# Kernel optimization log

Hardware: AMD Instinct MI355X
Metric: run time of the kernel (lower is better)

The kernel has to match this reference:

```python
import jax, jax.numpy as jnp
import numpy as np

N = 50000
E = 1600000
IN = 128
HID = 128
OUT = 64
NL = 200000
NEG_SLOPE = 0.2


def _glorot(key, shape):
    fan_in, fan_out = shape[0], shape[-1]
    s = jnp.sqrt(6.0 / (fan_in + fan_out))
    return jax.random.uniform(key, shape, jnp.float32, -s, s)


def setup_inputs() -> dict:
    key = jax.random.key(0)
    ks = jax.random.split(key, 16)
    x = jax.random.normal(ks[0], (N, IN), jnp.float32)
    edge_index = jax.random.randint(ks[1], (2, E), 0, N, dtype=jnp.int32)
    edge_label_index = jax.random.randint(ks[2], (2, NL), 0, N, dtype=jnp.int32)
    return {
        "x": x,
        "edge_index": edge_index,
        "edge_label_index": edge_label_index,
        "W1": _glorot(ks[3], (IN, HID)),  "a1s": _glorot(ks[4], (HID,)),  "a1d": _glorot(ks[5], (HID,)),  "b1": jnp.zeros((HID,), jnp.float32),
        "W2": _glorot(ks[6], (HID, HID)), "a2s": _glorot(ks[7], (HID,)),  "a2d": _glorot(ks[8], (HID,)),  "b2": jnp.zeros((HID,), jnp.float32),
        "W3": _glorot(ks[9], (HID, HID)), "a3s": _glorot(ks[10], (HID,)), "a3d": _glorot(ks[11], (HID,)), "b3": jnp.zeros((HID,), jnp.float32),
        "W4": _glorot(ks[12], (HID, OUT)), "b4": jnp.zeros((OUT,), jnp.float32),
    }


def _add_self_loops(edge_index, n):
    loop = jnp.arange(n, dtype=edge_index.dtype)
    return jnp.concatenate([edge_index, jnp.stack([loop, loop])], axis=1)


def gat_conv(x, edge_index, W, a_s, a_d, b):
    """PyG GATConv, heads=1, add_self_loops=True: gather, LeakyReLU score,
    segment softmax over destination nodes, scatter-add aggregate."""
    n = x.shape[0]
    ei = _add_self_loops(edge_index, n)
    src, dst = ei[0], ei[1]
    h = x @ W                                    # [N, H]
    e = jax.nn.leaky_relu((h @ a_s)[src] + (h @ a_d)[dst], NEG_SLOPE)  # [E']
    m = jax.ops.segment_max(e, dst, num_segments=n)
    p = jnp.exp(e - m[dst])
    s = jax.ops.segment_sum(p, dst, num_segments=n)
    alpha = p / s[dst]                           # segment softmax
    out = jax.ops.segment_sum(h[src] * alpha[:, None], dst, num_segments=n)
    return out + b


def gcn_conv(x, edge_index, W, b):
    """PyG GCNConv: self-loops + symmetric degree normalization."""
    n = x.shape[0]
    ei = _add_self_loops(edge_index, n)
    src, dst = ei[0], ei[1]
    h = x @ W
    deg = jax.ops.segment_sum(jnp.ones(src.shape, h.dtype), dst, num_segments=n)
    dinv = jax.lax.rsqrt(deg)
    norm = dinv[src] * dinv[dst]                 # [E']
    out = jax.ops.segment_sum(h[src] * norm[:, None], dst, num_segments=n)
    return out + b


def reference(x, edge_index, edge_label_index,
              W1, a1s, a1d, b1, W2, a2s, a2d, b2,
              W3, a3s, a3d, b3, W4, b4):
    h = jax.nn.relu(gat_conv(x, edge_index, W1, a1s, a1d, b1))
    h = jax.nn.relu(gat_conv(h, edge_index, W2, a2s, a2d, b2))
    h = jax.nn.relu(gat_conv(h, edge_index, W3, a3s, a3d, b3))
    z = gcn_conv(h, edge_index, W4, b4)          # [N, OUT]
    # decode: dot product of endpoint embeddings -> link logits [NL]
    return (z[edge_label_index[0]] * z[edge_label_index[1]]).sum(axis=-1)
```

## Files before the change

kernel.cpp:

```cpp
#include <hip/hip_runtime.h>
#include <hip/hip_fp16.h>
#include <math.h>

#define NN   50000
#define NE   1600000
#define DHID 128
#define DOUTC 64
#define NLBL 200000
#define CAP  80
#define NEG  0.2f
#define NBK  196
#define CAPB 8800
#define CHK  4096

typedef unsigned short u16;
typedef _Float16 half8 __attribute__((ext_vector_type(8)));
typedef float floatx4 __attribute__((ext_vector_type(4)));


__global__ __launch_bounds__(256) void k_zero(int* __restrict__ gcnt) {
    int i = threadIdx.x;
    if (i < NBK) gcnt[i] = 0;
}

__global__ __launch_bounds__(256) void k_bin(const int* __restrict__ ei,
                                             int* __restrict__ gcnt,
                                             unsigned* __restrict__ bins) {
    __shared__ int cntL[NBK];
    __shared__ int curL[NBK];
    const int tid = threadIdx.x;
    const int e0 = blockIdx.x * CHK + tid * 16;
    const bool act = (e0 + 15) < NE;

    unsigned pk[16];
    int bb[16];
    if (act) {
#pragma unroll
        for (int g = 0; g < 4; ++g) {
            int4 s4 = *(const int4*)&ei[e0 + g * 4];
            int4 d4 = *(const int4*)&ei[NE + e0 + g * 4];
            int sa[4] = {s4.x, s4.y, s4.z, s4.w};
            int da[4] = {d4.x, d4.y, d4.z, d4.w};
#pragma unroll
            for (int k = 0; k < 4; ++k) {
                int idx = g * 4 + k;
                bb[idx] = da[k] >> 8;
                pk[idx] = (unsigned)sa[k] | ((unsigned)(da[k] & 255) << 16);
            }
        }
    }
    for (int i = tid; i < NBK; i += 256) cntL[i] = 0;
    __syncthreads();
    if (act) {
#pragma unroll
        for (int k = 0; k < 16; ++k) atomicAdd(&cntL[bb[k]], 1);
    }
    __syncthreads();
    for (int i = tid; i < NBK; i += 256) curL[i] = atomicAdd(&gcnt[i], cntL[i]);
    __syncthreads();
    if (act) {
#pragma unroll
        for (int k = 0; k < 16; ++k) {
            int off = atomicAdd(&curL[bb[k]], 1);
            bins[(size_t)bb[k] * CAPB + off] = pk[k];
        }
    }
}

__global__ __launch_bounds__(256) void k_build(const unsigned* __restrict__ bins,
                                               const int* __restrict__ gcnt,
                                               int* __restrict__ cnt,
                                               u16* __restrict__ csr) {
    __shared__ u16 rows[256 * CAP];
    __shared__ int cur[256];
    const int b = blockIdx.x, tid = threadIdx.x;
    const int d0 = b << 8;
    const int nd = min(256, NN - d0);
    if (tid < nd) { cur[tid] = 1; rows[tid * CAP] = (u16)(d0 + tid); }
    __syncthreads();
    const int n = gcnt[b];
    for (int i = tid; i < n; i += 256) {
        unsigned v = bins[(size_t)b * CAPB + i];
        int s = v & 0xFFFF, dl = v >> 16;
        int pos = atomicAdd(&cur[dl], 1);
        if (pos < CAP) rows[dl * CAP + pos] = (u16)s;
    }
    __syncthreads();
    const unsigned* rw = (const unsigned*)rows;
    unsigned* cw = (unsigned*)(csr + (size_t)d0 * CAP);
    const int tot = nd * (CAP / 2);
    for (int i = tid; i < tot; i += 256) cw[i] = rw[i];
    if (tid < nd) cnt[d0 + tid] = cur[tid];
}


__global__ __launch_bounds__(256) void k_cast(const float* __restrict__ x,
                                              __half* __restrict__ x16) {
    int i = (blockIdx.x * 256 + threadIdx.x) * 4;
    if (i < NN * 128) {
        float4 v = *(const float4*)&x[i];
        __half2 h0 = __floats2half2_rn(v.x, v.y);
        __half2 h1 = __floats2half2_rn(v.z, v.w);
        uint2 u;
        __builtin_memcpy(&u.x, &h0, 4);
        __builtin_memcpy(&u.y, &h1, 4);
        *(uint2*)&x16[i] = u;
    }
}


__global__ __launch_bounds__(256) void k_prep_w(const float* __restrict__ W1f,
                                                const float* __restrict__ W2f,
                                                const float* __restrict__ W3f,
                                                const float* __restrict__ W4f,
                                                half8* __restrict__ Wf1,
                                                half8* __restrict__ Wf2,
                                                half8* __restrict__ Wf3,
                                                half8* __restrict__ Wf4) {
    int e = blockIdx.x * 256 + threadIdx.x;
    const float* W;
    half8* Wf;
    int nout, le;
    if (e < 2048)      { W = W1f; Wf = Wf1; nout = 128; le = e; }
    else if (e < 4096) { W = W2f; Wf = Wf2; nout = 128; le = e - 2048; }
    else if (e < 6144) { W = W3f; Wf = Wf3; nout = 128; le = e - 4096; }
    else if (e < 7168) { W = W4f; Wf = Wf4; nout = 64;  le = e - 6144; }
    else return;
    int c = le >> 8, rem = le & 255, ks = rem >> 6, lane = rem & 63;
    int n = lane & 15, quad = lane >> 4;
    int col = c * 16 + n, k0 = ks * 32 + quad * 8;
    half8 v;
#pragma unroll
    for (int j = 0; j < 8; ++j) v[j] = (_Float16)W[(size_t)(k0 + j) * nout + col];
    Wf[le] = v;
}


template <int NOUT, bool ATTN>
__global__ __launch_bounds__(256) void gemm_mfma(const __half* __restrict__ A16,
                                                 const half8* __restrict__ Wf,
                                                 __half* __restrict__ C16,
                                                 const float* __restrict__ a_s,
                                                 const float* __restrict__ a_d,
                                                 float* __restrict__ asv,
                                                 float* __restrict__ adv, int M) {
    constexpr int CT = NOUT / 16;
    const int tid = threadIdx.x;
    const int wave = tid >> 6, lane = tid & 63;
    const int n = lane & 15, quad = lane >> 4;
    const int row0 = blockIdx.x * 128 + wave * 32;

    half8 a[2][4];
    half8 zz = {};
#pragma unroll
    for (int t = 0; t < 2; ++t) {
        int row = row0 + t * 16 + n;
        const _Float16* Ap = (const _Float16*)A16 + (size_t)row * 128 + quad * 8;
        bool ok = row < M;
#pragma unroll
        for (int ks = 0; ks < 4; ++ks)
            a[t][ks] = ok ? *(const half8*)(Ap + ks * 32) : zz;
    }

    floatx4 acc[2][CT];
#pragma unroll
    for (int t = 0; t < 2; ++t)
#pragma unroll
        for (int c = 0; c < CT; ++c) acc[t][c] = (floatx4){0.f, 0.f, 0.f, 0.f};

#pragma unroll
    for (int c = 0; c < CT; ++c) {
#pragma unroll
        for (int ks = 0; ks < 4; ++ks) {
            half8 b = Wf[(c * 4 + ks) * 64 + lane];
            acc[0][c] = __builtin_amdgcn_mfma_f32_16x16x32_f16(b, a[0][ks], acc[0][c], 0, 0, 0);
            acc[1][c] = __builtin_amdgcn_mfma_f32_16x16x32_f16(b, a[1][ks], acc[1][c], 0, 0, 0);
        }
    }

#pragma unroll
    for (int t = 0; t < 2; ++t) {
        int row = row0 + t * 16 + n;
        if (row < M) {
#pragma unroll
            for (int c = 0; c < CT; ++c) {
                __half2 h0 = __floats2half2_rn(acc[t][c][0], acc[t][c][1]);
                __half2 h1 = __floats2half2_rn(acc[t][c][2], acc[t][c][3]);
                uint2 u;
                __builtin_memcpy(&u.x, &h0, 4);
                __builtin_memcpy(&u.y, &h1, 4);
                *(uint2*)&C16[(size_t)row * NOUT + c * 16 + quad * 4] = u;
            }
        }
    }

    if (ATTN) {
#pragma unroll
        for (int t = 0; t < 2; ++t) {
            float ps = 0.f, pd = 0.f;
#pragma unroll
            for (int c = 0; c < CT; ++c) {
#pragma unroll
                for (int reg = 0; reg < 4; ++reg) {
                    float w = acc[t][c][reg];
                    ps = fmaf(w, a_s[c * 16 + quad * 4 + reg], ps);
                    pd = fmaf(w, a_d[c * 16 + quad * 4 + reg], pd);
                }
            }
            ps += __shfl_xor(ps, 16); ps += __shfl_xor(ps, 32);
            pd += __shfl_xor(pd, 16); pd += __shfl_xor(pd, 32);
            int row = row0 + t * 16 + n;
            if (quad == 0 && row < M) { asv[row] = ps; adv[row] = pd; }
        }
    }
}

__device__ inline void fma_h8(uint4 u, float al, float* acc) {
    float2 f0 = __half22float2(*(__half2*)&u.x);
    float2 f1 = __half22float2(*(__half2*)&u.y);
    float2 f2 = __half22float2(*(__half2*)&u.z);
    float2 f3 = __half22float2(*(__half2*)&u.w);
    acc[0] = fmaf(al, f0.x, acc[0]);
    acc[1] = fmaf(al, f0.y, acc[1]);
    acc[2] = fmaf(al, f1.x, acc[2]);
    acc[3] = fmaf(al, f1.y, acc[3]);
    acc[4] = fmaf(al, f2.x, acc[4]);
    acc[5] = fmaf(al, f2.y, acc[5]);
    acc[6] = fmaf(al, f3.x, acc[6]);
    acc[7] = fmaf(al, f3.y, acc[7]);
}


__global__ __launch_bounds__(256) void k_gat_agg(const __half* __restrict__ h,
                                                 const int* __restrict__ cnt,
                                                 const u16* __restrict__ csr,
                                                 const float* __restrict__ asv,
                                                 const float* __restrict__ adv,
                                                 const float* __restrict__ bias,
                                                 __half* __restrict__ outp) {
    int lane = threadIdx.x & 63, wv = threadIdx.x >> 6;
    int d = blockIdx.x * 4 + wv;
    if (d >= NN) return;
    int deg = cnt[d]; if (deg > CAP) deg = CAP;
    const float advd = adv[d];
    const u16* rowp = csr + (size_t)d * CAP;

    int j0 = lane, j1 = lane + 64;
    int s0 = 0, s1 = 0;
    float e0 = -INFINITY, e1 = -INFINITY;
    if (j0 < deg) {
        s0 = rowp[j0];
        float t = asv[s0] + advd;
        e0 = (t >= 0.f) ? t : NEG * t;
    }
    if (j1 < deg) {
        s1 = rowp[j1];
        float t = asv[s1] + advd;
        e1 = (t >= 0.f) ? t : NEG * t;
    }
    float m = fmaxf(e0, e1);
#pragma unroll
    for (int off = 32; off; off >>= 1) m = fmaxf(m, __shfl_xor(m, off));
    float p0 = (j0 < deg) ? __expf(e0 - m) : 0.f;
    float p1 = (j1 < deg) ? __expf(e1 - m) : 0.f;
    float s = p0 + p1;
#pragma unroll
    for (int off = 32; off; off >>= 1) s += __shfl_xor(s, off);
    float inv = 1.f / s;
    float a0 = p0 * inv, a1 = p1 * inv;

    int slot = lane >> 3, r = lane & 7;
    float acc[16];
#pragma unroll
    for (int k = 0; k < 16; ++k) acc[k] = 0.f;

    for (int base = 0; base < deg; base += 8) {
        int idx = base + slot;
        int lsrc = idx & 63;
        float alA = __shfl(a0, lsrc);
        float alB = __shfl(a1, lsrc);
        int   sjA = __shfl(s0, lsrc);
        int   sjB = __shfl(s1, lsrc);
        bool ok = idx < deg;
        float al = ok ? ((idx < 64) ? alA : alB) : 0.f;
        int   sj = ok ? ((idx < 64) ? sjA : sjB) : 0;
        const uint4* hp = (const uint4*)&h[(size_t)sj * 128 + r * 16];
        uint4 ua = hp[0];
        uint4 ub = hp[1];
        fma_h8(ua, al, acc);
        fma_h8(ub, al, acc + 8);
    }
#pragma unroll
    for (int k = 0; k < 16; ++k) {
        acc[k] += __shfl_xor(acc[k], 8);
        acc[k] += __shfl_xor(acc[k], 16);
        acc[k] += __shfl_xor(acc[k], 32);
    }
    if (slot == 0) {
        __half2 ho[8];
#pragma unroll
        for (int k = 0; k < 8; ++k) {
            float oa = fmaxf(acc[2 * k]     + bias[r * 16 + 2 * k],     0.f);
            float ob = fmaxf(acc[2 * k + 1] + bias[r * 16 + 2 * k + 1], 0.f);
            ho[k] = __floats2half2_rn(oa, ob);
        }
        uint4 u0, u1;
        __builtin_memcpy(&u0, &ho[0], 16);
        __builtin_memcpy(&u1, &ho[4], 16);
        uint4* op = (uint4*)&outp[(size_t)d * 128 + r * 16];
        op[0] = u0; op[1] = u1;
    }
}


__global__ __launch_bounds__(256) void k_gcn_agg(const __half* __restrict__ h,
                                                 const int* __restrict__ cnt,
                                                 const u16* __restrict__ csr,
                                                 const float* __restrict__ bias,
                                                 float* __restrict__ z) {
    int lane = threadIdx.x & 63, wv = threadIdx.x >> 6;
    int d = blockIdx.x * 4 + wv;
    if (d >= NN) return;
    int degc = cnt[d];
    int deg = degc > CAP ? CAP : degc;
    float did = rsqrtf((float)degc);
    const u16* rowp = csr + (size_t)d * CAP;

    int j0 = lane, j1 = lane + 64;
    int s0 = 0, s1 = 0;
    float n0 = 0.f, n1 = 0.f;
    if (j0 < deg) { s0 = rowp[j0]; n0 = rsqrtf((float)cnt[s0]) * did; }
    if (j1 < deg) { s1 = rowp[j1]; n1 = rsqrtf((float)cnt[s1]) * did; }

    int slot = lane >> 3, r = lane & 7;
    float acc[8];
#pragma unroll
    for (int k = 0; k < 8; ++k) acc[k] = 0.f;

    for (int base = 0; base < deg; base += 8) {
        int idx = base + slot;
        int lsrc = idx & 63;
        float nA = __shfl(n0, lsrc);
        float nB = __shfl(n1, lsrc);
        int  sjA = __shfl(s0, lsrc);
        int  sjB = __shfl(s1, lsrc);
        bool ok = idx < deg;
        float nm = ok ? ((idx < 64) ? nA : nB) : 0.f;
        int   sj = ok ? ((idx < 64) ? sjA : sjB) : 0;
        uint4 u = *(const uint4*)&h[(size_t)sj * 64 + r * 8];
        fma_h8(u, nm, acc);
    }
#pragma unroll
    for (int k = 0; k < 8; ++k) {
        acc[k] += __shfl_xor(acc[k], 8);
        acc[k] += __shfl_xor(acc[k], 16);
        acc[k] += __shfl_xor(acc[k], 32);
    }
    if (slot == 0) {
        float4 b0 = *(const float4*)&bias[r * 8];
        float4 b1 = *(const float4*)&bias[r * 8 + 4];
        float4* zp = (float4*)&z[(size_t)d * 64 + r * 8];
        zp[0] = make_float4(acc[0] + b0.x, acc[1] + b0.y, acc[2] + b0.z, acc[3] + b0.w);
        zp[1] = make_float4(acc[4] + b1.x, acc[5] + b1.y, acc[6] + b1.z, acc[7] + b1.w);
    }
}


__global__ __launch_bounds__(256) void k_decode(const float* __restrict__ z,
                                                const int* __restrict__ eli,
                                                float* __restrict__ outp) {
    int lane = threadIdx.x & 63, wv = threadIdx.x >> 6;
    int g = lane >> 4, r = lane & 15;
    int idx = (blockIdx.x * 4 + wv) * 4 + g;
    if (idx >= NLBL) return;
    int a = eli[idx], b = eli[NLBL + idx];
    float4 za = *(const float4*)&z[(size_t)a * 64 + r * 4];
    float4 zb = *(const float4*)&z[(size_t)b * 64 + r * 4];
    float v = za.x * zb.x + za.y * zb.y + za.z * zb.z + za.w * zb.w;
#pragma unroll
    for (int off = 8; off; off >>= 1) v += __shfl_xor(v, off);
    if (r == 0) outp[idx] = v;
}


extern "C" void kernel_launch(void* const* d_in, const int* in_sizes, int n_in,
                              void* d_out, int out_size, void* d_ws, size_t ws_size,
                              hipStream_t stream) {
    const float* x   = (const float*)d_in[0];
    const int*   ei  = (const int*)d_in[1];
    const int*   eli = (const int*)d_in[2];
    const float* W1 = (const float*)d_in[3];
    const float* a1s = (const float*)d_in[4];
    const float* a1d = (const float*)d_in[5];
    const float* b1 = (const float*)d_in[6];
    const float* W2 = (const float*)d_in[7];
    const float* a2s = (const float*)d_in[8];
    const float* a2d = (const float*)d_in[9];
    const float* b2 = (const float*)d_in[10];
    const float* W3 = (const float*)d_in[11];
    const float* a3s = (const float*)d_in[12];
    const float* a3d = (const float*)d_in[13];
    const float* b3 = (const float*)d_in[14];
    const float* W4 = (const float*)d_in[15];
    const float* b4 = (const float*)d_in[16];
    float* outp = (float*)d_out;

    char* p = (char*)d_ws;
    auto alloc = [&](size_t bytes) -> char* {
        char* r = p;
        p += (bytes + 255) & ~(size_t)255;
        return r;
    };
    int*    cnt  = (int*)alloc((size_t)NN * 4);
    u16*    csr  = (u16*)alloc((size_t)NN * CAP * 2);
    int*    gcnt = (int*)alloc((size_t)NBK * 4);
    float*  asv  = (float*)alloc((size_t)NN * 4);
    float*  advv = (float*)alloc((size_t)NN * 4);
    __half* x16  = (__half*)alloc((size_t)NN * 128 * 2);
    __half* G    = (__half*)alloc((size_t)NN * 128 * 2);
    __half* Bu1  = (__half*)alloc((size_t)NN * 128 * 2);
    __half* Bu2  = (__half*)alloc((size_t)NN * 128 * 2);
    float*  zf   = (float*)alloc((size_t)NN * 64 * 4);
    half8*  Wf1  = (half8*)alloc(2048 * 16);
    half8*  Wf2  = (half8*)alloc(2048 * 16);
    half8*  Wf3  = (half8*)alloc(2048 * 16);
    half8*  Wf4  = (half8*)alloc(1024 * 16);
    unsigned* bins = (unsigned*)alloc((size_t)NBK * CAPB * 4);

    const int gBin  = (NE + CHK - 1) / CHK;
    const int gCast = (NN * 128 / 4 + 255) / 256;
    const int gGemm = (NN + 127) / 128;
    const int gNode = (NN + 3) / 4;
    const int gDec  = (NLBL + 15) / 16;

    k_zero<<<1, 256, 0, stream>>>(gcnt);
    k_bin<<<gBin, 256, 0, stream>>>(ei, gcnt, bins);
    k_build<<<NBK, 256, 0, stream>>>(bins, gcnt, cnt, csr);
    k_cast<<<gCast, 256, 0, stream>>>(x, x16);
    k_prep_w<<<28, 256, 0, stream>>>(W1, W2, W3, W4, Wf1, Wf2, Wf3, Wf4);

    gemm_mfma<128, true><<<gGemm, 256, 0, stream>>>(x16, Wf1, G, a1s, a1d, asv, advv, NN);
    k_gat_agg<<<gNode, 256, 0, stream>>>(G, cnt, csr, asv, advv, b1, Bu1);

    gemm_mfma<128, true><<<gGemm, 256, 0, stream>>>(Bu1, Wf2, G, a2s, a2d, asv, advv, NN);
    k_gat_agg<<<gNode, 256, 0, stream>>>(G, cnt, csr, asv, advv, b2, Bu2);

    gemm_mfma<128, true><<<gGemm, 256, 0, stream>>>(Bu2, Wf3, G, a3s, a3d, asv, advv, NN);
    k_gat_agg<<<gNode, 256, 0, stream>>>(G, cnt, csr, asv, advv, b3, Bu1);

    gemm_mfma<64, false><<<gGemm, 256, 0, stream>>>(Bu1, Wf4, G, nullptr, nullptr, nullptr, nullptr, NN);
    k_gcn_agg<<<gNode, 256, 0, stream>>>(G, cnt, csr, b4, zf);

    k_decode<<<gDec, 256, 0, stream>>>(zf, eli, outp);
}
```

Baseline: 430.2 us.

## Fuse cast into first GEMM, merge zero kernel, use LDS edge lists, fp16 z

The fp32→fp16 cast of x moves into the first GEMM through a templated input type, and the gcnt zeroing is folded into k_prep_w as an extra block, which removes two launches and one full pass over x. The GEMM now does 16 rows per wave instead of 32, which doubles the grid and reduces register pressure. The GAT and GCN aggregations stage per-edge alpha/norm and source indices in LDS instead of using per-iteration shuffles. The final embedding z is stored in fp16, halving decode gather traffic at some precision cost.

```diff
diff --git a/kernel.cpp b/kernel.cpp
--- a/kernel.cpp
+++ b/kernel.cpp
@@ -17,11 +17,6 @@
 typedef _Float16 half8 __attribute__((ext_vector_type(8)));
 typedef float floatx4 __attribute__((ext_vector_type(4)));
 
-
-__global__ __launch_bounds__(256) void k_zero(int* __restrict__ gcnt) {
-    int i = threadIdx.x;
-    if (i < NBK) gcnt[i] = 0;
-}
 
 __global__ __launch_bounds__(256) void k_bin(const int* __restrict__ ei,
                                              int* __restrict__ gcnt,
@@ -94,21 +89,6 @@
 }
 
 
-__global__ __launch_bounds__(256) void k_cast(const float* __restrict__ x,
-                                              __half* __restrict__ x16) {
-    int i = (blockIdx.x * 256 + threadIdx.x) * 4;
-    if (i < NN * 128) {
-        float4 v = *(const float4*)&x[i];
-        __half2 h0 = __floats2half2_rn(v.x, v.y);
-        __half2 h1 = __floats2half2_rn(v.z, v.w);
-        uint2 u;
-        __builtin_memcpy(&u.x, &h0, 4);
-        __builtin_memcpy(&u.y, &h1, 4);
-        *(uint2*)&x16[i] = u;
-    }
-}
-
-
 __global__ __launch_bounds__(256) void k_prep_w(const float* __restrict__ W1f,
                                                 const float* __restrict__ W2f,
                                                 const float* __restrict__ W3f,
@@ -116,7 +96,13 @@
                                                 half8* __restrict__ Wf1,
                                                 half8* __restrict__ Wf2,
                                                 half8* __restrict__ Wf3,
-                                                half8* __restrict__ Wf4) {
+                                                half8* __restrict__ Wf4,
+                                                int* __restrict__ gcnt) {
+    if (blockIdx.x == 28) {
+        int i = threadIdx.x;
+        if (i < NBK) gcnt[i] = 0;
+        return;
+    }
     int e = blockIdx.x * 256 + threadIdx.x;
     const float* W;
     half8* Wf;
@@ -124,8 +110,7 @@
     if (e < 2048)      { W = W1f; Wf = Wf1; nout = 128; le = e; }
     else if (e < 4096) { W = W2f; Wf = Wf2; nout = 128; le = e - 2048; }
     else if (e < 6144) { W = W3f; Wf = Wf3; nout = 128; le = e - 4096; }
-    else if (e < 7168) { W = W4f; Wf = Wf4; nout = 64;  le = e - 6144; }
-    else return;
+    else               { W = W4f; Wf = Wf4; nout = 64;  le = e - 6144; }
     int c = le >> 8, rem = le & 255, ks = rem >> 6, lane = rem & 63;
     int n = lane & 15, quad = lane >> 4;
     int col = c * 16 + n, k0 = ks * 32 + quad * 8;
@@ -136,8 +121,8 @@
 }
 
 
-template <int NOUT, bool ATTN>
-__global__ __launch_bounds__(256) void gemm_mfma(const __half* __restrict__ A16,
+template <int NOUT, bool ATTN, typename TA>
+__global__ __launch_bounds__(256) void gemm_mfma(const TA* __restrict__ Ain,
                                                  const half8* __restrict__ Wf,
                                                  __half* __restrict__ C16,
                                                  const float* __restrict__ a_s,
@@ -148,70 +133,67 @@
     const int tid = threadIdx.x;
     const int wave = tid >> 6, lane = tid & 63;
     const int n = lane & 15, quad = lane >> 4;
-    const int row0 = blockIdx.x * 128 + wave * 32;
-
-    half8 a[2][4];
+    const int row0 = blockIdx.x * 64 + wave * 16;
+
+    const int row = row0 + n;
+    const bool ok = row < M;
+    half8 a[4];
     half8 zz = {};
 #pragma unroll
-    for (int t = 0; t < 2; ++t) {
-        int row = row0 + t * 16 + n;
-        const _Float16* Ap = (const _Float16*)A16 + (size_t)row * 128 + quad * 8;
-        bool ok = row < M;
-#pragma unroll
-        for (int ks = 0; ks < 4; ++ks)
-            a[t][ks] = ok ? *(const half8*)(Ap + ks * 32) : zz;
-    }
-
-    floatx4 acc[2][CT];
-#pragma unroll
-    for (int t = 0; t < 2; ++t)
-#pragma unroll
-        for (int c = 0; c < CT; ++c) acc[t][c] = (floatx4){0.f, 0.f, 0.f, 0.f};
+    for (int ks = 0; ks < 4; ++ks) {
+        if (!ok) { a[ks] = zz; continue; }
+        if constexpr (sizeof(TA) == 2) {
+            a[ks] = *(const half8*)((const _Float16*)Ain + (size_t)row * 128 + quad * 8 + ks * 32);
+        } else {
+            const float* Ap = (const float*)Ain + (size_t)row * 128 + quad * 8 + ks * 32;
+            float4 f0 = *(const float4*)Ap;
+            float4 f1 = *(const float4*)(Ap + 4);
+            half8 v;
+            v[0] = (_Float16)f0.x; v[1] = (_Float16)f0.y; v[2] = (_Float16)f0.z; v[3] = (_Float16)f0.w;
+            v[4] = (_Float16)f1.x; v[5] = (_Float16)f1.y; v[6] = (_Float16)f1.z; v[7] = (_Float16)f1.w;
+            a[ks] = v;
+        }
+    }
+
+    floatx4 acc[CT];
+#pragma unroll
+    for (int c = 0; c < CT; ++c) acc[c] = (floatx4){0.f, 0.f, 0.f, 0.f};
 
 #pragma unroll
     for (int c = 0; c < CT; ++c) {
 #pragma unroll
         for (int ks = 0; ks < 4; ++ks) {
             half8 b = Wf[(c * 4 + ks) * 64 + lane];
-            acc[0][c] = __builtin_amdgcn_mfma_f32_16x16x32_f16(b, a[0][ks], acc[0][c], 0, 0, 0);
-            acc[1][c] = __builtin_amdgcn_mfma_f32_16x16x32_f16(b, a[1][ks], acc[1][c], 0, 0, 0);
-        }
-    }
-
-#pragma unroll
-    for (int t = 0; t < 2; ++t) {
-        int row = row0 + t * 16 + n;
-        if (row < M) {
-#pragma unroll
-            for (int c = 0; c < CT; ++c) {
-                __half2 h0 = __floats2half2_rn(acc[t][c][0], acc[t][c][1]);
-                __half2 h1 = __floats2half2_rn(acc[t][c][2], acc[t][c][3]);
-                uint2 u;
-                __builtin_memcpy(&u.x, &h0, 4);
-                __builtin_memcpy(&u.y, &h1, 4);
-                *(uint2*)&C16[(size_t)row * NOUT + c * 16 + quad * 4] = u;
+            acc[c] = __builtin_amdgcn_mfma_f32_16x16x32_f16(b, a[ks], acc[c], 0, 0, 0);
+        }
+    }
+
+    if (ok) {
+#pragma unroll
+        for (int c = 0; c < CT; ++c) {
+            __half2 h0 = __floats2half2_rn(acc[c][0], acc[c][1]);
+            __half2 h1 = __floats2half2_rn(acc[c][2], acc[c][3]);
+            uint2 u;
+            __builtin_memcpy(&u.x, &h0, 4);
+            __builtin_memcpy(&u.y, &h1, 4);
+            *(uint2*)&C16[(size_t)row * NOUT + c * 16 + quad * 4] = u;
+        }
+    }
+
+    if (ATTN) {
+        float ps = 0.f, pd = 0.f;
+#pragma unroll
+        for (int c = 0; c < CT; ++c) {
+#pragma unroll
+            for (int reg = 0; reg < 4; ++reg) {
+                float w = acc[c][reg];
+                ps = fmaf(w, a_s[c * 16 + quad * 4 + reg], ps);
+                pd = fmaf(w, a_d[c * 16 + quad * 4 + reg], pd);
             }
         }
-    }
-
-    if (ATTN) {
-#pragma unroll
-        for (int t = 0; t < 2; ++t) {
-            float ps = 0.f, pd = 0.f;
-#pragma unroll
-            for (int c = 0; c < CT; ++c) {
-#pragma unroll
-                for (int reg = 0; reg < 4; ++reg) {
-                    float w = acc[t][c][reg];
-                    ps = fmaf(w, a_s[c * 16 + quad * 4 + reg], ps);
-                    pd = fmaf(w, a_d[c * 16 + quad * 4 + reg], pd);
-                }
-            }
-            ps += __shfl_xor(ps, 16); ps += __shfl_xor(ps, 32);
-            pd += __shfl_xor(pd, 16); pd += __shfl_xor(pd, 32);
-            int row = row0 + t * 16 + n;
-            if (quad == 0 && row < M) { asv[row] = ps; adv[row] = pd; }
-        }
+        ps += __shfl_xor(ps, 16); ps += __shfl_xor(ps, 32);
+        pd += __shfl_xor(pd, 16); pd += __shfl_xor(pd, 32);
+        if (quad == 0 && ok) { asv[row] = ps; adv[row] = pd; }
     }
 }
 
@@ -238,6 +220,8 @@
                                                  const float* __restrict__ adv,
                                                  const float* __restrict__ bias,
                                                  __half* __restrict__ outp) {
+    __shared__ float alsL[4][88];
+    __shared__ int   srcL[4][88];
     int lane = threadIdx.x & 63, wv = threadIdx.x >> 6;
     int d = blockIdx.x * 4 + wv;
     if (d >= NN) return;
@@ -267,23 +251,20 @@
 #pragma unroll
     for (int off = 32; off; off >>= 1) s += __shfl_xor(s, off);
     float inv = 1.f / s;
-    float a0 = p0 * inv, a1 = p1 * inv;
+    alsL[wv][j0] = p0 * inv;
+    srcL[wv][j0] = s0;
+    if (j1 < 88) { alsL[wv][j1] = p1 * inv; srcL[wv][j1] = s1; }
 
     int slot = lane >> 3, r = lane & 7;
     float acc[16];
 #pragma unroll
     for (int k = 0; k < 16; ++k) acc[k] = 0.f;
 
-    for (int base = 0; base < deg; base += 8) {
+    int degp = (deg + 7) & ~7;
+    for (int base = 0; base < degp; base += 8) {
         int idx = base + slot;
-        int lsrc = idx & 63;
-        float alA = __shfl(a0, lsrc);
-        float alB = __shfl(a1, lsrc);
-        int   sjA = __shfl(s0, lsrc);
-        int   sjB = __shfl(s1, lsrc);
-        bool ok = idx < deg;
-        float al = ok ? ((idx < 64) ? alA : alB) : 0.f;
-        int   sj = ok ? ((idx < 64) ? sjA : sjB) : 0;
+        float al = alsL[wv][idx];
+        int   sj = srcL[wv][idx];
         const uint4* hp = (const uint4*)&h[(size_t)sj * 128 + r * 16];
         uint4 ua = hp[0];
         uint4 ub = hp[1];
@@ -317,7 +298,9 @@
                                                  const int* __restrict__ cnt,
                                                  const u16* __restrict__ csr,
                                                  const float* __restrict__ bias,
-                                                 float* __restrict__ z) {
+                                                 __half* __restrict__ z) {
+    __shared__ float nmL[4][88];
+    __shared__ int   srcL[4][88];
     int lane = threadIdx.x & 63, wv = threadIdx.x >> 6;
     int d = blockIdx.x * 4 + wv;
     if (d >= NN) return;
@@ -331,22 +314,20 @@
     float n0 = 0.f, n1 = 0.f;
     if (j0 < deg) { s0 = rowp[j0]; n0 = rsqrtf((float)cnt[s0]) * did; }
     if (j1 < deg) { s1 = rowp[j1]; n1 = rsqrtf((float)cnt[s1]) * did; }
+    nmL[wv][j0] = n0;
+    srcL[wv][j0] = s0;
+    if (j1 < 88) { nmL[wv][j1] = n1; srcL[wv][j1] = s1; }
 
     int slot = lane >> 3, r = lane & 7;
     float acc[8];
 #pragma unroll
     for (int k = 0; k < 8; ++k) acc[k] = 0.f;
 
-    for (int base = 0; base < deg; base += 8) {
+    int degp = (deg + 7) & ~7;
+    for (int base = 0; base < degp; base += 8) {
         int idx = base + slot;
-        int lsrc = idx & 63;
-        float nA = __shfl(n0, lsrc);
-        float nB = __shfl(n1, lsrc);
-        int  sjA = __shfl(s0, lsrc);
-        int  sjB = __shfl(s1, lsrc);
-        bool ok = idx < deg;
-        float nm = ok ? ((idx < 64) ? nA : nB) : 0.f;
-        int   sj = ok ? ((idx < 64) ? sjA : sjB) : 0;
+        float nm = nmL[wv][idx];
+        int   sj = srcL[wv][idx];
         uint4 u = *(const uint4*)&h[(size_t)sj * 64 + r * 8];
         fma_h8(u, nm, acc);
     }
@@ -357,16 +338,23 @@
         acc[k] += __shfl_xor(acc[k], 32);
     }
     if (slot == 0) {
-        float4 b0 = *(const float4*)&bias[r * 8];
-        float4 b1 = *(const float4*)&bias[r * 8 + 4];
-        float4* zp = (float4*)&z[(size_t)d * 64 + r * 8];
-        zp[0] = make_float4(acc[0] + b0.x, acc[1] + b0.y, acc[2] + b0.z, acc[3] + b0.w);
-        zp[1] = make_float4(acc[4] + b1.x, acc[5] + b1.y, acc[6] + b1.z, acc[7] + b1.w);
-    }
-}
-
-
-__global__ __launch_bounds__(256) void k_decode(const float* __restrict__ z,
+        __half2 ho[4];
+#pragma unroll
+        for (int k = 0; k < 4; ++k) {
+            float oa = acc[2 * k]     + bias[r * 8 + 2 * k];
+            float ob = acc[2 * k + 1] + bias[r * 8 + 2 * k + 1];
+            ho[k] = __floats2half2_rn(oa, ob);
+        }
+        uint2 u0, u1;
+        __builtin_memcpy(&u0, &ho[0], 8);
+        __builtin_memcpy(&u1, &ho[2], 8);
+        uint2* zp = (uint2*)&z[(size_t)d * 64 + r * 8];
+        zp[0] = u0; zp[1] = u1;
+    }
+}
+
+
+__global__ __launch_bounds__(256) void k_decode(const __half* __restrict__ z,
                                                 const int* __restrict__ eli,
                                                 float* __restrict__ outp) {
     int lane = threadIdx.x & 63, wv = threadIdx.x >> 6;
@@ -374,9 +362,13 @@
     int idx = (blockIdx.x * 4 + wv) * 4 + g;
     if (idx >= NLBL) return;
     int a = eli[idx], b = eli[NLBL + idx];
-    float4 za = *(const float4*)&z[(size_t)a * 64 + r * 4];
-    float4 zb = *(const float4*)&z[(size_t)b * 64 + r * 4];
-    float v = za.x * zb.x + za.y * zb.y + za.z * zb.z + za.w * zb.w;
+    uint2 ua = *(const uint2*)&z[(size_t)a * 64 + r * 4];
+    uint2 ub = *(const uint2*)&z[(size_t)b * 64 + r * 4];
+    float2 a0 = __half22float2(*(__half2*)&ua.x);
+    float2 a1 = __half22float2(*(__half2*)&ua.y);
+    float2 b0 = __half22float2(*(__half2*)&ub.x);
+    float2 b1 = __half22float2(*(__half2*)&ub.y);
+    float v = a0.x * b0.x + a0.y * b0.y + a1.x * b1.x + a1.y * b1.y;
 #pragma unroll
     for (int off = 8; off; off >>= 1) v += __shfl_xor(v, off);
     if (r == 0) outp[idx] = v;
@@ -416,11 +408,10 @@
     int*    gcnt = (int*)alloc((size_t)NBK * 4);
     float*  asv  = (float*)alloc((size_t)NN * 4);
     float*  advv = (float*)alloc((size_t)NN * 4);
-    __half* x16  = (__half*)alloc((size_t)NN * 128 * 2);
     __half* G    = (__half*)alloc((size_t)NN * 128 * 2);
     __half* Bu1  = (__half*)alloc((size_t)NN * 128 * 2);
     __half* Bu2  = (__half*)alloc((size_t)NN * 128 * 2);
-    float*  zf   = (float*)alloc((size_t)NN * 64 * 4);
+    __half* zf   = (__half*)alloc((size_t)NN * 64 * 2);
     half8*  Wf1  = (half8*)alloc(2048 * 16);
     half8*  Wf2  = (half8*)alloc(2048 * 16);
     half8*  Wf3  = (half8*)alloc(2048 * 16);
@@ -428,27 +419,24 @@
     unsigned* bins = (unsigned*)alloc((size_t)NBK * CAPB * 4);
 
     const int gBin  = (NE + CHK - 1) / CHK;
-    const int gCast = (NN * 128 / 4 + 255) / 256;
-    const int gGemm = (NN + 127) / 128;
+    const int gGemm = (NN + 63) / 64;
     const int gNode = (NN + 3) / 4;
     const int gDec  = (NLBL + 15) / 16;
 
-    k_zero<<<1, 256, 0, stream>>>(gcnt);
+    k_prep_w<<<29, 256, 0, stream>>>(W1, W2, W3, W4, Wf1, Wf2, Wf3, Wf4, gcnt);
     k_bin<<<gBin, 256, 0, stream>>>(ei, gcnt, bins);
     k_build<<<NBK, 256, 0, stream>>>(bins, gcnt, cnt, csr);
-    k_cast<<<gCast, 256, 0, stream>>>(x, x16);
-    k_prep_w<<<28, 256, 0, stream>>>(W1, W2, W3, W4, Wf1, Wf2, Wf3, Wf4);
-
-    gemm_mfma<128, true><<<gGemm, 256, 0, stream>>>(x16, Wf1, G, a1s, a1d, asv, advv, NN);
+
+    gemm_mfma<128, true, float><<<gGemm, 256, 0, stream>>>(x, Wf1, G, a1s, a1d, asv, advv, NN);
     k_gat_agg<<<gNode, 256, 0, stream>>>(G, cnt, csr, asv, advv, b1, Bu1);
 
-    gemm_mfma<128, true><<<gGemm, 256, 0, stream>>>(Bu1, Wf2, G, a2s, a2d, asv, advv, NN);
+    gemm_mfma<128, true, __half><<<gGemm, 256, 0, stream>>>(Bu1, Wf2, G, a2s, a2d, asv, advv, NN);
     k_gat_agg<<<gNode, 256, 0, stream>>>(G, cnt, csr, asv, advv, b2, Bu2);
 
-    gemm_mfma<128, true><<<gGemm, 256, 0, stream>>>(Bu2, Wf3, G, a3s, a3d, asv, advv, NN);
+    gemm_mfma<128, true, __half><<<gGemm, 256, 0, stream>>>(Bu2, Wf3, G, a3s, a3d, asv, advv, NN);
     k_gat_agg<<<gNode, 256, 0, stream>>>(G, cnt, csr, asv, advv, b3, Bu1);
 
-    gemm_mfma<64, false><<<gGemm, 256, 0, stream>>>(Bu1, Wf4, G, nullptr, nullptr, nullptr, nullptr, NN);
+    gemm_mfma<64, false, __half><<<gGemm, 256, 0, stream>>>(Bu1, Wf4, G, nullptr, nullptr, nullptr, nullptr, NN);
     k_gcn_agg<<<gNode, 256, 0, stream>>>(G, cnt, csr, b4, zf);
 
     k_decode<<<gDec, 256, 0, stream>>>(zf, eli, outp);
```

New measurement: 398.7 us. 7.3% less time.
